# Optimization experiments

Hardware: AMD Instinct MI355X
Metric: run time of the kernel (lower is better)

The kernel has to match this reference:

```python
import jax, jax.numpy as jnp
import numpy as np


def setup_inputs() -> dict:
    key = jax.random.key(0)
    k1, k2 = jax.random.split(key)
    B, C, N = 2, 3, 16384
    in_pc = jax.random.normal(k1, (B, C, N), dtype=jnp.float32)
    target_pc = jax.random.normal(k2, (B, C, N), dtype=jnp.float32)
    return {"in_pc": in_pc, "target_pc": target_pc}


def reference(in_pc, target_pc):
    # [B,3,N] -> [B,N,3]
    pc1 = jnp.transpose(in_pc, (0, 2, 1))
    pc2 = jnp.transpose(target_pc, (0, 2, 1))
    sqr = (-2.0 * jnp.einsum('bnc,bmc->bnm', pc1, pc2)
           + jnp.sum(pc1 ** 2, -1)[:, :, None]
           + jnp.sum(pc2 ** 2, -1)[:, None, :])
    dist1 = jnp.min(sqr, axis=-1)  # [B,N] NN from pc1 to pc2
    dist2 = jnp.min(sqr, axis=1)   # [B,M] NN from pc2 to pc1
    m_dist = (dist1 + dist2) / 2.0  # requires N == M (as in original)
    return jnp.mean(m_dist)
```

## Files before the change

kernel.cpp:

```cpp
#include <hip/hip_runtime.h>

#define BLK 512
#define MT 32
#define IB 256
#define TJQ 512
#define SJ 4

typedef __attribute__((ext_vector_type(8))) short short8;
typedef __attribute__((ext_vector_type(16))) float f32x16;

__device__ __forceinline__ unsigned int fmap(float f) {
  unsigned int b = __float_as_uint(f);
  return (b & 0x80000000u) ? ~b : (b | 0x80000000u);
}
__device__ __forceinline__ float funmap(unsigned int u) {
  return __uint_as_float((u & 0x80000000u) ? (u ^ 0x80000000u) : ~u);
}
__device__ __forceinline__ unsigned short f2bf(float f) {
  unsigned int u = __float_as_uint(f);
  u += 0x7FFFu + ((u >> 16) & 1u);
  return (unsigned short)(u >> 16);
}
__device__ __forceinline__ float bf2f(unsigned short h) {
  return __uint_as_float(((unsigned int)h) << 16);
}
__device__ __forceinline__ unsigned int pk(unsigned short a, unsigned short b) {
  return (unsigned int)a | ((unsigned int)b << 16);
}

union FragU { uint4 u; short8 s; };

__global__ __launch_bounds__(BLK, 4) void cl_mfma(
    const float* __restrict__ A, const float* __restrict__ Bp,
    unsigned int* __restrict__ umin, int N, int jslice, int Bn) {
  __shared__ uint4 sA[2][IB];
  __shared__ uint4 sB[2][TJQ];
  __shared__ float sNP[IB];

  const int zi = blockIdx.z;
  const int dir = zi / Bn;
  const int b = zi - dir * Bn;
  const float* __restrict__ P = dir ? Bp : A;
  const float* __restrict__ Q = dir ? A : Bp;
  unsigned int* __restrict__ um = umin + ((size_t)dir * Bn + b) * N;

  const int t = threadIdx.x;
  const int ib0 = blockIdx.x * IB;
  const int jbase = blockIdx.y * jslice;
  const size_t boff = (size_t)b * 3 * N;
  const unsigned short one = 0x3F80u;

  if (t < IB) {
    int i = ib0 + t;
    float x = P[boff + i], y = P[boff + N + i], zz = P[boff + 2 * N + i];
    float ax = -2.f * x, ay = -2.f * y, az = -2.f * zz;
    unsigned short hx = f2bf(ax), hy = f2bf(ay), hz = f2bf(az);
    unsigned short lx = f2bf(ax - bf2f(hx)), ly = f2bf(ay - bf2f(hy)),
                   lz = f2bf(az - bf2f(hz));
    sA[0][t] = make_uint4(pk(hx, hy), pk(hz, lx), pk(ly, lz), pk(hx, hy));
    sA[1][t] = make_uint4(pk(hz, lx), pk(ly, lz), pk(one, one), pk(one, 0));
    sNP[t] = fmaf(zz, zz, fmaf(y, y, x * x));
  }
  __syncthreads();

  const int w = t >> 6, l = t & 63, m = l & 31, g = l >> 5;
  FragU au; au.u = sA[g][w * MT + m];
  const short8 af = au.s;

  f32x16 run, zc;
#pragma unroll
  for (int r = 0; r < 16; ++r) { run[r] = 3.0e38f; zc[r] = 0.0f; }

  const int nch = jslice / TJQ;
  float qx = Q[boff + jbase + t];
  float qy = Q[boff + N + jbase + t];
  float qz = Q[boff + 2 * N + jbase + t];

  for (int ch = 0; ch < nch; ++ch) {
    unsigned short hx = f2bf(qx), hy = f2bf(qy), hz = f2bf(qz);
    unsigned short lx = f2bf(qx - bf2f(hx)), ly = f2bf(qy - bf2f(hy)),
                   lz = f2bf(qz - bf2f(hz));
    float nq = fmaf(qz, qz, fmaf(qy, qy, qx * qx));
    unsigned short nh = f2bf(nq);
    float r1 = nq - bf2f(nh);
    unsigned short nm = f2bf(r1);
    unsigned short nl = f2bf(r1 - bf2f(nm));
    uint4 b0 = make_uint4(pk(hx, hy), pk(hz, hx), pk(hy, hz), pk(lx, ly));
    uint4 b1 = make_uint4(pk(lz, lx), pk(ly, lz), pk(nh, nm), pk(nl, 0));

    __syncthreads();
    sB[0][t] = b0;
    sB[1][t] = b1;
    {
      int jn = (ch + 1 < nch) ? (jbase + (ch + 1) * TJQ + t) : (jbase + t);
      qx = Q[boff + jn];
      qy = Q[boff + N + jn];
      qz = Q[boff + 2 * N + jn];
    }
    __syncthreads();

#pragma unroll 2
    for (int jt = 0; jt < TJQ / MT; jt += 2) {
      FragU ba, bb;
      ba.u = sB[g][jt * MT + m];
      bb.u = sB[g][(jt + 1) * MT + m];
      f32x16 da = __builtin_amdgcn_mfma_f32_32x32x16_bf16(af, ba.s, zc, 0, 0, 0);
      f32x16 db = __builtin_amdgcn_mfma_f32_32x32x16_bf16(af, bb.s, zc, 0, 0, 0);
#pragma unroll
      for (int r = 0; r < 16; ++r)
        run[r] = fminf(fminf(run[r], da[r]), db[r]);
    }
  }

#pragma unroll
  for (int r = 0; r < 16; ++r) {
    float v = run[r];
    v = fminf(v, __shfl_xor(v, 1));
    v = fminf(v, __shfl_xor(v, 2));
    v = fminf(v, __shfl_xor(v, 4));
    v = fminf(v, __shfl_xor(v, 8));
    v = fminf(v, __shfl_xor(v, 16));
    if (m == 0) {
      int row = (r & 3) + 8 * (r >> 2) + 4 * g;
      int il = w * MT + row;
      atomicMin(&um[ib0 + il], fmap(v + sNP[il]));
    }
  }
}

__global__ __launch_bounds__(1024) void cl_reduce(
    const unsigned int* __restrict__ u, float* __restrict__ out, int total) {
  const int t = threadIdx.x;
  const uint4* __restrict__ u4 = (const uint4*)u;
  double s = 0.0;
  for (int i = t; i < total / 4; i += 1024) {
    uint4 v = u4[i];
    s += (double)funmap(v.x) + (double)funmap(v.y) +
         (double)funmap(v.z) + (double)funmap(v.w);
  }
  for (int off = 32; off > 0; off >>= 1) s += __shfl_down(s, off, 64);
  __shared__ double sw[16];
  if ((t & 63) == 0) sw[t >> 6] = s;
  __syncthreads();
  if (t == 0) {
    double tot = 0.0;
    for (int wv = 0; wv < 16; ++wv) tot += sw[wv];
    out[0] = (float)(tot / (double)total);
  }
}

extern "C" void kernel_launch(void* const* d_in, const int* in_sizes, int n_in,
                              void* d_out, int out_size, void* d_ws, size_t ws_size,
                              hipStream_t stream) {
  const float* in_pc = (const float*)d_in[0];
  const float* tgt_pc = (const float*)d_in[1];
  const int B = 2, N = 16384;
  unsigned int* u = (unsigned int*)d_ws;
  float* out = (float*)d_out;

  hipMemsetAsync(u, 0xFF, (size_t)2 * B * N * sizeof(unsigned int), stream);

  const int jslice = N / SJ;
  dim3 grid(N / IB, SJ, 2 * B);
  cl_mfma<<<grid, dim3(BLK), 0, stream>>>(in_pc, tgt_pc, u, N, jslice, B);

  const int total = 2 * B * N;
  cl_reduce<<<dim3(1), dim3(1024), 0, stream>>>(u, out, total);
}
```

Before: 104.8 us.

## Give each wave two A row-tiles to reuse B fragments across MFMAs

Each wave now keeps two 32-row A fragments and applies each loaded B fragment to both, which halves LDS reads of B per MFMA. IB grows to 512 and SJ to 8 so the grid stays balanced. The inner loop is fully unrolled and asm barriers pin the MFMA results in VGPRs. Doubling the running-min registers drops the occupancy target from 4 to 2 blocks per CU, which trades latency hiding for more reuse.

```diff
diff --git a/kernel.cpp b/kernel.cpp
--- a/kernel.cpp
+++ b/kernel.cpp
@@ -2,12 +2,15 @@
 
 #define BLK 512
 #define MT 32
-#define IB 256
+#define IA 2
+#define IB 512
 #define TJQ 512
-#define SJ 4
+#define SJ 8
 
 typedef __attribute__((ext_vector_type(8))) short short8;
 typedef __attribute__((ext_vector_type(16))) float f32x16;
+
+#define FORCE_V(x) asm volatile("" : "+v"(x))
 
 __device__ __forceinline__ unsigned int fmap(float f) {
   unsigned int b = __float_as_uint(f);
@@ -30,7 +33,7 @@
 
 union FragU { uint4 u; short8 s; };
 
-__global__ __launch_bounds__(BLK, 4) void cl_mfma(
+__global__ __launch_bounds__(BLK, 2) void cl_mfma(
     const float* __restrict__ A, const float* __restrict__ Bp,
     unsigned int* __restrict__ umin, int N, int jslice, int Bn) {
   __shared__ uint4 sA[2][IB];
@@ -50,7 +53,7 @@
   const size_t boff = (size_t)b * 3 * N;
   const unsigned short one = 0x3F80u;
 
-  if (t < IB) {
+  {
     int i = ib0 + t;
     float x = P[boff + i], y = P[boff + N + i], zz = P[boff + 2 * N + i];
     float ax = -2.f * x, ay = -2.f * y, az = -2.f * zz;
@@ -64,12 +67,16 @@
   __syncthreads();
 
   const int w = t >> 6, l = t & 63, m = l & 31, g = l >> 5;
-  FragU au; au.u = sA[g][w * MT + m];
-  const short8 af = au.s;
+  FragU a0u, a1u;
+  a0u.u = sA[g][w * (MT * IA) + m];
+  a1u.u = sA[g][w * (MT * IA) + MT + m];
+  const short8 af0 = a0u.s, af1 = a1u.s;
 
-  f32x16 run, zc;
+  float run0[16], run1[16];
+  f32x16 zc;
 #pragma unroll
-  for (int r = 0; r < 16; ++r) { run[r] = 3.0e38f; zc[r] = 0.0f; }
+  for (int r = 0; r < 16; ++r) { run0[r] = 3.0e38f; run1[r] = 3.0e38f; zc[r] = 0.0f; }
+  FORCE_V(zc);
 
   const int nch = jslice / TJQ;
   float qx = Q[boff + jbase + t];
@@ -85,12 +92,12 @@
     float r1 = nq - bf2f(nh);
     unsigned short nm = f2bf(r1);
     unsigned short nl = f2bf(r1 - bf2f(nm));
-    uint4 b0 = make_uint4(pk(hx, hy), pk(hz, hx), pk(hy, hz), pk(lx, ly));
-    uint4 b1 = make_uint4(pk(lz, lx), pk(ly, lz), pk(nh, nm), pk(nl, 0));
+    uint4 b0s = make_uint4(pk(hx, hy), pk(hz, hx), pk(hy, hz), pk(lx, ly));
+    uint4 b1s = make_uint4(pk(lz, lx), pk(ly, lz), pk(nh, nm), pk(nl, 0));
 
     __syncthreads();
-    sB[0][t] = b0;
-    sB[1][t] = b1;
+    sB[0][t] = b0s;
+    sB[1][t] = b1s;
     {
       int jn = (ch + 1 < nch) ? (jbase + (ch + 1) * TJQ + t) : (jbase + t);
       qx = Q[boff + jn];
@@ -99,31 +106,40 @@
     }
     __syncthreads();
 
-#pragma unroll 2
+#pragma unroll
     for (int jt = 0; jt < TJQ / MT; jt += 2) {
       FragU ba, bb;
-      ba.u = sB[g][jt * MT + m];
+      ba.u = sB[g][(jt + 0) * MT + m];
       bb.u = sB[g][(jt + 1) * MT + m];
-      f32x16 da = __builtin_amdgcn_mfma_f32_32x32x16_bf16(af, ba.s, zc, 0, 0, 0);
-      f32x16 db = __builtin_amdgcn_mfma_f32_32x32x16_bf16(af, bb.s, zc, 0, 0, 0);
+      f32x16 d0 = __builtin_amdgcn_mfma_f32_32x32x16_bf16(af0, ba.s, zc, 0, 0, 0);
+      f32x16 d1 = __builtin_amdgcn_mfma_f32_32x32x16_bf16(af0, bb.s, zc, 0, 0, 0);
+      FORCE_V(d0); FORCE_V(d1);
 #pragma unroll
       for (int r = 0; r < 16; ++r)
-        run[r] = fminf(fminf(run[r], da[r]), db[r]);
+        run0[r] = fminf(fminf(run0[r], d0[r]), d1[r]);
+      f32x16 d2 = __builtin_amdgcn_mfma_f32_32x32x16_bf16(af1, ba.s, zc, 0, 0, 0);
+      f32x16 d3 = __builtin_amdgcn_mfma_f32_32x32x16_bf16(af1, bb.s, zc, 0, 0, 0);
+      FORCE_V(d2); FORCE_V(d3);
+#pragma unroll
+      for (int r = 0; r < 16; ++r)
+        run1[r] = fminf(fminf(run1[r], d2[r]), d3[r]);
     }
   }
 
 #pragma unroll
   for (int r = 0; r < 16; ++r) {
-    float v = run[r];
-    v = fminf(v, __shfl_xor(v, 1));
-    v = fminf(v, __shfl_xor(v, 2));
-    v = fminf(v, __shfl_xor(v, 4));
-    v = fminf(v, __shfl_xor(v, 8));
-    v = fminf(v, __shfl_xor(v, 16));
+    float v0 = run0[r], v1 = run1[r];
+#pragma unroll
+    for (int sh = 1; sh <= 16; sh <<= 1) {
+      v0 = fminf(v0, __shfl_xor(v0, sh));
+      v1 = fminf(v1, __shfl_xor(v1, sh));
+    }
     if (m == 0) {
       int row = (r & 3) + 8 * (r >> 2) + 4 * g;
-      int il = w * MT + row;
-      atomicMin(&um[ib0 + il], fmap(v + sNP[il]));
+      int il0 = w * (MT * IA) + row;
+      int il1 = il0 + MT;
+      atomicMin(&um[ib0 + il0], fmap(v0 + sNP[il0]));
+      atomicMin(&um[ib0 + il1], fmap(v1 + sNP[il1]));
     }
   }
 }
```

Result: slower. 114.1 us (+8.9%).
